# Kernel optimization log

Measured on AMD Instinct MI355X. Metric: run time of the kernel, lower is better.

The kernel has to match this reference:

```python
import jax, jax.numpy as jnp
import numpy as np

T_DIFF = 1000.0
LN_EPS = 1e-5


def _lin(x, w, b):
    return jnp.matmul(x, w.T) + b


def _ln(x, g, b):
    m = jnp.mean(x, axis=-1, keepdims=True)
    v = jnp.mean((x - m) ** 2, axis=-1, keepdims=True)
    return (x - m) / jnp.sqrt(v + LN_EPS) * g + b


def _pos_lin(x, w, b):
    return jnp.matmul(x, jax.nn.softplus(w).T) + b


def _gamma(t, g_l1_w, g_l1_b, g_l2_w, g_l2_b, g_l3_w, g_l3_b, gamma_0, gamma_1):
    def gtilde(u):
        l1 = _pos_lin(u, g_l1_w, g_l1_b)
        return l1 + _pos_lin(jax.nn.sigmoid(_pos_lin(l1, g_l2_w, g_l2_b)), g_l3_w, g_l3_b)
    g0, g1, gt = gtilde(jnp.zeros_like(t)), gtilde(jnp.ones_like(t)), gtilde(t)
    return gamma_0 + (gamma_1 - gamma_0) * (gt - g0) / (g1 - g0)


def _pair_dist(a):
    # safe pairwise euclidean distances, (B,N,N,1)
    diff = a[:, :, None, :] - a[:, None, :, :]
    d2 = jnp.sum(diff * diff, axis=-1, keepdims=True)
    return diff, jnp.sqrt(jnp.maximum(d2, 1e-12)), d2


def _egc_layer(x, h, x0, p):
    _, d0, _ = _pair_dist(x0)                      # original distances
    diff, dist, d2 = _pair_dist(x)                 # current distances (pre-LN x)
    h = _ln(h, p['lnh_g'], p['lnh_b'])
    x = _ln(x, p['lnx_g'], p['lnx_b'])
    B, N, F = h.shape
    h_i = jnp.broadcast_to(h[:, :, None, :], (B, N, N, F))
    h_j = jnp.broadcast_to(h[:, None, :, :], (B, N, N, F))
    einp = jnp.concatenate([h_i, h_j, d2, d0], axis=-1)  # (B,N,N,2F+2)
    m = jax.nn.silu(_lin(einp, p['edg1_w'], p['edg1_b']))
    m = jax.nn.silu(_lin(m, p['edg2_w'], p['edg2_b']))
    e = jax.nn.sigmoid(_lin(m, p['edgi_w'], p['edgi_b']))
    e = e * (1.0 - jnp.eye(N, dtype=e.dtype)[None, :, :, None])
    m_agg = jnp.sum(e * m, axis=2)                 # sum over j -> (B,N,F)
    hn = jax.nn.silu(_lin(jnp.concatenate([h, m_agg], axis=-1), p['node1_w'], p['node1_b']))
    hn = h + _lin(hn, p['node2_w'], p['node2_b'])
    cw = jax.nn.silu(_lin(einp, p['cor1_w'], p['cor1_b']))
    cw = jax.nn.silu(_lin(cw, p['cor2_w'], p['cor2_b']))
    cw = _lin(cw, p['cor3_w'], p['cor3_b'])        # (B,N,N,1)
    x_next = x + jnp.sum(cw * (diff / (dist + 1.0)), axis=2)
    return x_next, hn


def setup_inputs() -> dict:
    key = jax.random.key(0)
    ks = iter(jax.random.split(key, 64))
    B, N, H, L = 8, 192, 32, 4
    d = {}
    d['xyz_atom_species'] = jax.random.normal(next(ks), (B, N, 4), jnp.float32)
    d['pdf'] = jax.random.normal(next(ks), (B, 3000), jnp.float32)
    d['t'] = jax.random.uniform(next(ks), (B,), jnp.float32) * T_DIFF

    def w(k, shape):
        fan_in = shape[-1]
        return jax.random.normal(k, shape, jnp.float32) / np.sqrt(fan_in)

    d['emb_in_w'] = w(next(ks), (H, 12)); d['emb_in_b'] = jnp.zeros((H,), jnp.float32)
    d['emb_out_w'] = w(next(ks), (1, H)); d['emb_out_b'] = jnp.zeros((1,), jnp.float32)
    d['x_out_w'] = w(next(ks), (3, 3)); d['x_out_b'] = jnp.zeros((3,), jnp.float32)
    d['pdf_w'] = w(next(ks), (10, 3000)); d['pdf_b'] = jnp.zeros((10,), jnp.float32)
    d['g_l1_w'] = w(next(ks), (1, 1)); d['g_l1_b'] = jnp.zeros((1,), jnp.float32)
    d['g_l2_w'] = w(next(ks), (1024, 1)); d['g_l2_b'] = jnp.zeros((1024,), jnp.float32)
    d['g_l3_w'] = w(next(ks), (1, 1024)); d['g_l3_b'] = jnp.zeros((1,), jnp.float32)
    d['gamma_0'] = jnp.array([-5.0], jnp.float32)
    d['gamma_1'] = jnp.array([10.0], jnp.float32)
    d['lnh_g'] = jnp.ones((L, H), jnp.float32); d['lnh_b'] = jnp.zeros((L, H), jnp.float32)
    d['lnx_g'] = jnp.ones((L, 3), jnp.float32); d['lnx_b'] = jnp.zeros((L, 3), jnp.float32)
    d['edg1_w'] = w(next(ks), (L, H, 2 * H + 2)); d['edg1_b'] = jnp.zeros((L, H), jnp.float32)
    d['edg2_w'] = w(next(ks), (L, H, H)); d['edg2_b'] = jnp.zeros((L, H), jnp.float32)
    d['edgi_w'] = w(next(ks), (L, 1, H)); d['edgi_b'] = jnp.zeros((L, 1), jnp.float32)
    d['node1_w'] = w(next(ks), (L, H, 2 * H)); d['node1_b'] = jnp.zeros((L, H), jnp.float32)
    d['node2_w'] = w(next(ks), (L, H, H)); d['node2_b'] = jnp.zeros((L, H), jnp.float32)
    d['cor1_w'] = w(next(ks), (L, H, 2 * H + 2)); d['cor1_b'] = jnp.zeros((L, H), jnp.float32)
    d['cor2_w'] = w(next(ks), (L, H, H)); d['cor2_b'] = jnp.zeros((L, H), jnp.float32)
    d['cor3_w'] = w(next(ks), (L, 1, H)); d['cor3_b'] = jnp.zeros((L, 1), jnp.float32)
    return d


def reference(xyz_atom_species, pdf, t, emb_in_w, emb_in_b, emb_out_w, emb_out_b,
              x_out_w, x_out_b, pdf_w, pdf_b, g_l1_w, g_l1_b, g_l2_w, g_l2_b,
              g_l3_w, g_l3_b, gamma_0, gamma_1, lnh_g, lnh_b, lnx_g, lnx_b,
              edg1_w, edg1_b, edg2_w, edg2_b, edgi_w, edgi_b, node1_w, node1_b,
              node2_w, node2_b, cor1_w, cor1_b, cor2_w, cor2_b, cor3_w, cor3_b):
    B, N, _ = xyz_atom_species.shape
    h = xyz_atom_species[:, :, 3:4]                # (B,N,1)
    x = xyz_atom_species[:, :, :3]
    x0 = x
    tn = (t / T_DIFF)[:, None]                     # (B,1)
    t_emb = _gamma(tn, g_l1_w, g_l1_b, g_l2_w, g_l2_b, g_l3_w, g_l3_b, gamma_0, gamma_1)
    pdf_emb = _lin(pdf, pdf_w, pdf_b)              # (B,10)
    h = jnp.concatenate([
        h,
        jnp.broadcast_to(t_emb[:, None, :], (B, N, 1)),
        jnp.broadcast_to(pdf_emb[:, None, :], (B, N, 10)),
    ], axis=-1)
    h = _lin(h, emb_in_w, emb_in_b)                # (B,N,32)
    for l in range(4):
        p = dict(lnh_g=lnh_g[l], lnh_b=lnh_b[l], lnx_g=lnx_g[l], lnx_b=lnx_b[l],
                 edg1_w=edg1_w[l], edg1_b=edg1_b[l], edg2_w=edg2_w[l], edg2_b=edg2_b[l],
                 edgi_w=edgi_w[l], edgi_b=edgi_b[l], node1_w=node1_w[l], node1_b=node1_b[l],
                 node2_w=node2_w[l], node2_b=node2_b[l], cor1_w=cor1_w[l], cor1_b=cor1_b[l],
                 cor2_w=cor2_w[l], cor2_b=cor2_b[l], cor3_w=cor3_w[l], cor3_b=cor3_b[l])
        x, h = _egc_layer(x, h, x0, p)
    h = _lin(h, emb_out_w, emb_out_b)
    x = _lin(x, x_out_w, x_out_b) - x0
    return jnp.concatenate([x, h], axis=-1)        # (B,N,4)
```

## Files before the change

### kernel.cpp

```cpp
#include <hip/hip_runtime.h>
#include <hip/hip_bf16.h>
#include <math.h>

#define BATCH 8
#define NATOMS 192

using short8 = __attribute__((ext_vector_type(8))) short;
using f32x4  = __attribute__((ext_vector_type(4))) float;

__device__ __forceinline__ float fast_rcp(float x){ return __builtin_amdgcn_rcpf(x); }
__device__ __forceinline__ float sigmoid_f(float x){ return fast_rcp(1.0f+__expf(-x)); }
__device__ __forceinline__ float silu_f(float x){ return x*fast_rcp(1.0f+__expf(-x)); }
__device__ __forceinline__ float softplus_f(float x){ return fmaxf(x,0.0f)+log1pf(expf(-fabsf(x))); }
__device__ __forceinline__ unsigned short f2bf(float x){
  __hip_bfloat16 h = __float2bfloat16(x);
  return __builtin_bit_cast(unsigned short, h);
}

__device__ __forceinline__ float wave_sum(float v){
  v += __shfl_xor(v, 1);
  v += __shfl_xor(v, 2);
  v += __shfl_xor(v, 4);
  v += __shfl_xor(v, 8);
  v += __shfl_xor(v, 16);
  v += __shfl_xor(v, 32);
  return v;
}
__device__ __forceinline__ float sum32(float v){
  v += __shfl_xor(v, 1);
  v += __shfl_xor(v, 2);
  v += __shfl_xor(v, 4);
  v += __shfl_xor(v, 8);
  v += __shfl_xor(v, 16);
  return v;
}
__device__ __forceinline__ float sum16(float v){
  v += __shfl_xor(v, 1);
  v += __shfl_xor(v, 2);
  v += __shfl_xor(v, 4);
  v += __shfl_xor(v, 8);
  return v;
}

struct KP {
  const float *xyz, *pdf, *t;
  const float *emb_in_w, *emb_in_b, *emb_out_w, *emb_out_b, *x_out_w, *x_out_b;
  const float *pdf_w, *pdf_b;
  const float *g1w, *g1b, *g2w, *g2b, *g3w, *g3b, *gamma0, *gamma1;
  const float *lnhg, *lnhb, *lnxg, *lnxb;
  const float *e1w, *e1b, *e2w, *e2b, *eiw, *eib;
  const float *n1w, *n1b, *n2w, *n2b;
  const float *c1w, *c1b, *c2w, *c2b, *c3w, *c3b;
  float *temb, *pdfe;
  unsigned short *e2wb, *c2wb;
  float *hln0, *hln1, *ue0, *uc0, *vep0, *vcp0, *ue1, *uc1, *vep1, *vcp1;
  float *xb0, *xb1;
  float *out;
};

__global__ __launch_bounds__(128) void k_prelude(KP P)
{
  __shared__ float s_sm[8];
  const int bx = blockIdx.x, tid = threadIdx.x;
  const int wv = tid >> 6, ln = tid & 63;

  if (bx < 80){
    const int b = bx / 10, o = bx % 10;
    const float* pb = P.pdf + b*3000;
    const float* wb = P.pdf_w + o*3000;
    float p = 0.f;
    for (int k = tid; k < 3000; k += 128) p = fmaf(pb[k], wb[k], p);
    p = wave_sum(p);
    if (ln == 0) s_sm[wv] = p;
    __syncthreads();
    if (tid == 0) P.pdfe[b*10 + o] = s_sm[0] + s_sm[1] + P.pdf_b[o];
  } else if (bx < 88){
    const int b = bx - 80;
    const float w1 = softplus_f(P.g1w[0]);
    const float b1 = P.g1b[0];
    const float tn = P.t[b] * (1.0f/1000.0f);
    const float l1_0 = b1;
    const float l1_1 = w1 + b1;
    const float l1_t = fmaf(w1, tn, b1);
    float a0 = 0.f, a1 = 0.f, at = 0.f;
    for (int k = tid; k < 1024; k += 128){
      float w2 = softplus_f(P.g2w[k]);
      float bb = P.g2b[k];
      float w3 = softplus_f(P.g3w[k]);
      a0 += sigmoid_f(fmaf(w2, l1_0, bb)) * w3;
      a1 += sigmoid_f(fmaf(w2, l1_1, bb)) * w3;
      at += sigmoid_f(fmaf(w2, l1_t, bb)) * w3;
    }
    float vals[3] = {a0, a1, at};
#pragma unroll
    for (int r = 0; r < 3; ++r){
      float v = wave_sum(vals[r]);
      if (ln == 0) s_sm[r*2 + wv] = v;
    }
    __syncthreads();
    if (tid == 0){
      const float b3 = P.g3b[0];
      const float g0  = l1_0 + s_sm[0] + s_sm[1] + b3;
      const float g1v = l1_1 + s_sm[2] + s_sm[3] + b3;
      const float gt  = l1_t + s_sm[4] + s_sm[5] + b3;
      P.temb[b] = P.gamma0[0] + (P.gamma1[0] - P.gamma0[0]) * (gt - g0) / (g1v - g0);
    }
  } else {
    const int g = (bx - 88)*128 + tid;
    P.e2wb[g] = f2bf(P.e2w[g]);
    P.c2wb[g] = f2bf(P.c2w[g]);
  }
}

__global__ __launch_bounds__(128) void k_embed(KP P)
{
  __shared__ float s_hl[32];
  const int nid = blockIdx.x;
  const int tid = threadIdx.x;
  const int wv = tid >> 6, ln = tid & 63;
  const int b = nid / NATOMS;
  if (tid < 32){
    const int f = tid;
    const float* w = P.emb_in_w + f*12;
    float a = P.emb_in_b[f];
    a = fmaf(P.xyz[nid*4 + 3], w[0], a);
    a = fmaf(P.temb[b], w[1], a);
    const float* pe = P.pdfe + b*10;
#pragma unroll
    for (int q = 0; q < 10; ++q) a = fmaf(pe[q], w[2+q], a);
    const float m = sum32(a) * (1.0f/32.0f);
    const float d = a - m;
    const float v = sum32(d*d);
    const float r = rsqrtf(v*(1.0f/32.0f) + 1e-5f);
    const float hlv = fmaf(d*r, P.lnhg[f], P.lnhb[f]);
    s_hl[f] = hlv;
    P.hln0[(size_t)nid*32 + f] = hlv;
    if (f < 3) P.xb0[(size_t)nid*3 + f] = P.xyz[nid*4 + f];
  }
  __syncthreads();
  if (ln < 32){
    const int f = ln;
    const float* W = ((wv == 0) ? P.e1w : P.c1w) + f*66;
    float sv = ((wv == 0) ? P.e1b : P.c1b)[f], su = 0.f;
#pragma unroll
    for (int k = 0; k < 32; ++k){ sv = fmaf(s_hl[k], W[k], sv); su = fmaf(s_hl[k], W[32+k], su); }
    if (wv == 0){ P.vep0[(size_t)nid*32 + f] = sv; P.ue0[(size_t)nid*32 + f] = su; }
    else        { P.vcp0[(size_t)nid*32 + f] = sv; P.uc0[(size_t)nid*32 + f] = su; }
  }
}

__global__ __launch_bounds__(256, 4) void k_layer(KP P, int l, int last,
    const float* __restrict__ xcur, float* __restrict__ xnxt,
    const float* __restrict__ hlnC, float* __restrict__ hlnN,
    const float* __restrict__ ueC, const float* __restrict__ ucC,
    const float* __restrict__ vepC, const float* __restrict__ vcpC,
    float* __restrict__ ueN, float* __restrict__ ucN,
    float* __restrict__ vepN, float* __restrict__ vcpN)
{
  __shared__ float s_geo[192][6];
  __shared__ float s_mgp[2][32];
  __shared__ float s_pxp[2][4];
  __shared__ float s_hv[32];
  __shared__ float s_n1[32];
  __shared__ float s_hl[32];

  const int nid = blockIdx.x;
  const int b = nid / NATOMS;
  const int i = nid - b*NATOMS;
  const int base = b*NATOMS;
  const int tid = threadIdx.x;
  const int wv = tid >> 6, lane = tid & 63;
  const int n16 = lane & 15, quad = lane >> 4;
  const int is_edge = (wv < 2);
  const int half = wv & 1;

  {
    const float* xi_p = xcur + (size_t)nid*3;
    const float xi0 = xi_p[0], xi1 = xi_p[1], xi2 = xi_p[2];
    const float* x0i = P.xyz + (size_t)nid*4;
    const float q0i = x0i[0], q1i = x0i[1], q2i = x0i[2];
    for (int j = tid; j < NATOMS; j += 256){
      const float* xj_p = xcur + (size_t)(base + j)*3;
      const float dfx = xi0 - xj_p[0], dfy = xi1 - xj_p[1], dfz = xi2 - xj_p[2];
      const float d2 = dfx*dfx + dfy*dfy + dfz*dfz;
      const float dist = sqrtf(fmaxf(d2, 1e-12f));
      const float* x0j = P.xyz + (size_t)(base + j)*4;
      const float q0 = q0i - x0j[0], q1 = q1i - x0j[1], q2 = q2i - x0j[2];
      const float d0 = sqrtf(fmaxf(q0*q0 + q1*q1 + q2*q2, 1e-12f));
      s_geo[j][0] = dfx; s_geo[j][1] = dfy; s_geo[j][2] = dfz;
      s_geo[j][3] = d2;  s_geo[j][4] = d0;  s_geo[j][5] = dist;
    }
  }

  const float* e1wl = (is_edge ? P.e1w : P.c1w) + l*2112;
  const float* vp   = (is_edge ? vepC : vcpC) + (size_t)nid*32;
  const float* uu   = is_edge ? ueC : ucC;
  const unsigned short* w2b = (is_edge ? P.e2wb : P.c2wb) + l*1024;
  const float* bias2 = (is_edge ? P.e2b : P.c2b) + l*32;
  const float* wout  = (is_edge ? P.eiw : P.c3w) + l*32;
  const float  bout  = (is_edge ? P.eib : P.c3b)[l];

  float vp8[8], wA[8], wB[8];
#pragma unroll
  for (int q = 0; q < 8; ++q){
    const int k = quad*8 + q;
    vp8[q] = vp[k];
    wA[q] = e1wl[k*66 + 64];
    wB[q] = e1wl[k*66 + 65];
  }
  const short8 wb0 = *(const short8*)(w2b + n16*32 + quad*8);
  const short8 wb1 = *(const short8*)(w2b + 512 + n16*32 + quad*8);

  float bA[4], bB[4], wAo[4], wBo[4];
#pragma unroll
  for (int r = 0; r < 4; ++r){
    bA[r]  = bias2[quad*4 + r];
    bB[r]  = bias2[16 + quad*4 + r];
    wAo[r] = wout[quad*4 + r];
    wBo[r] = wout[16 + quad*4 + r];
  }

  __syncthreads();

  float acc0[4] = {0.f,0.f,0.f,0.f};
  float acc1[4] = {0.f,0.f,0.f,0.f};
  float px = 0.f, py = 0.f, pz = 0.f;

#pragma unroll 3
  for (int t = half; t < 12; t += 2){
    const int j = t*16 + n16;
    const float d2 = s_geo[j][3], d0 = s_geo[j][4];
    const float* ur = uu + (size_t)(base + j)*32 + quad*8;
    const f32x4 ua = *(const f32x4*)ur;
    const f32x4 ub = *(const f32x4*)(ur + 4);
    short8 a;
#pragma unroll
    for (int q = 0; q < 4; ++q)
      a[q] = (short)f2bf(silu_f(fmaf(d2, wA[q], fmaf(d0, wB[q], vp8[q] + ua[q]))));
#pragma unroll
    for (int q = 0; q < 4; ++q)
      a[4+q] = (short)f2bf(silu_f(fmaf(d2, wA[4+q], fmaf(d0, wB[4+q], vp8[4+q] + ub[q]))));

    const f32x4 z = {0.f, 0.f, 0.f, 0.f};
    const f32x4 A0 = __builtin_amdgcn_mfma_f32_16x16x32_bf16(wb0, a, z, 0, 0, 0);
    const f32x4 A1 = __builtin_amdgcn_mfma_f32_16x16x32_bf16(wb1, a, z, 0, 0, 0);

    float m20[4], m21[4];
#pragma unroll
    for (int r = 0; r < 4; ++r){
      m20[r] = silu_f(A0[r] + bA[r]);
      m21[r] = silu_f(A1[r] + bB[r]);
    }
    float gp = 0.f;
#pragma unroll
    for (int r = 0; r < 4; ++r) gp += m20[r]*wAo[r] + m21[r]*wBo[r];
    gp += __shfl_xor(gp, 16);
    gp += __shfl_xor(gp, 32);

    if (is_edge){
      const float e = (j == i) ? 0.0f : sigmoid_f(gp + bout);
#pragma unroll
      for (int r = 0; r < 4; ++r){
        acc0[r] = fmaf(e, m20[r], acc0[r]);
        acc1[r] = fmaf(e, m21[r], acc1[r]);
      }
    } else {
      const float s = (gp + bout) * fast_rcp(s_geo[j][5] + 1.0f);
      px = fmaf(s, s_geo[j][0], px);
      py = fmaf(s, s_geo[j][1], py);
      pz = fmaf(s, s_geo[j][2], pz);
    }
  }

  if (is_edge){
#pragma unroll
    for (int r = 0; r < 4; ++r){
      acc0[r] = sum16(acc0[r]);
      acc1[r] = sum16(acc1[r]);
    }
    if (n16 == 0){
#pragma unroll
      for (int r = 0; r < 4; ++r){
        s_mgp[half][quad*4 + r] = acc0[r];
        s_mgp[half][16 + quad*4 + r] = acc1[r];
      }
    }
  } else {
    px = sum16(px); py = sum16(py); pz = sum16(pz);
    if (lane == 0){
      s_pxp[half][0] = px; s_pxp[half][1] = py; s_pxp[half][2] = pz;
    }
    if (half == 1 && lane < 32) s_hv[lane] = hlnC[(size_t)nid*32 + lane];
  }
  __syncthreads();

  if (wv == 0){
    if (lane < 32){
      const int f = lane;
      float a = P.n1b[l*32 + f];
      const float* w1 = P.n1w + l*2048 + f*64;
#pragma unroll
      for (int k = 0; k < 32; ++k) a = fmaf(s_hv[k], w1[k], a);
#pragma unroll
      for (int k = 0; k < 32; ++k) a = fmaf(s_mgp[0][k] + s_mgp[1][k], w1[32+k], a);
      s_n1[f] = silu_f(a);
    }
  } else if (wv == 1){
    const float tx = s_pxp[0][0] + s_pxp[1][0];
    const float ty = s_pxp[0][1] + s_pxp[1][1];
    const float tz = s_pxp[0][2] + s_pxp[1][2];
    const float* xr = xcur + (size_t)nid*3;
    const float x0 = xr[0], x1 = xr[1], x2 = xr[2];
    const float mx = (x0 + x1 + x2) * (1.0f/3.0f);
    const float v0 = x0-mx, v1 = x1-mx, v2 = x2-mx;
    const float r = rsqrtf((v0*v0 + v1*v1 + v2*v2)*(1.0f/3.0f) + 1e-5f);
    const float xn0 = fmaf((x0 - mx)*r, P.lnxg[l*3+0], P.lnxb[l*3+0]) + tx;
    const float xn1 = fmaf((x1 - mx)*r, P.lnxg[l*3+1], P.lnxb[l*3+1]) + ty;
    const float xn2 = fmaf((x2 - mx)*r, P.lnxg[l*3+2], P.lnxb[l*3+2]) + tz;
    if (!last){
      if (lane == 0){
        float* xo = xnxt + (size_t)nid*3;
        xo[0] = xn0; xo[1] = xn1; xo[2] = xn2;
      }
    } else if (lane < 3){
      const float xn[3] = {xn0, xn1, xn2};
      float o = P.x_out_b[lane];
      o = fmaf(xn[0], P.x_out_w[lane*3 + 0], o);
      o = fmaf(xn[1], P.x_out_w[lane*3 + 1], o);
      o = fmaf(xn[2], P.x_out_w[lane*3 + 2], o);
      P.out[(size_t)nid*4 + lane] = o - P.xyz[(size_t)nid*4 + lane];
    }
  }
  __syncthreads();

  if (wv == 0 && lane < 32){
    const int f = lane;
    float o = P.n2b[l*32 + f];
    const float* w2 = P.n2w + l*1024 + f*32;
#pragma unroll
    for (int k = 0; k < 32; ++k) o = fmaf(s_n1[k], w2[k], o);
    const float ho = s_hv[f] + o;
    if (last){
      float hp = sum32(ho * P.emb_out_w[f]);
      if (f == 0) P.out[(size_t)nid*4 + 3] = hp + P.emb_out_b[0];
    } else {
      const int nx = l + 1;
      const float m = sum32(ho) * (1.0f/32.0f);
      const float d = ho - m;
      const float v = sum32(d*d);
      const float r = rsqrtf(v*(1.0f/32.0f) + 1e-5f);
      const float hlv = fmaf(d*r, P.lnhg[nx*32 + f], P.lnhb[nx*32 + f]);
      s_hl[f] = hlv;
      hlnN[(size_t)nid*32 + f] = hlv;
    }
  }
  if (!last){
    __syncthreads();
    if (wv < 2 && lane < 32){
      const int f = lane;
      const int nx = l + 1;
      const float* W = ((wv == 0) ? P.e1w : P.c1w) + nx*2112 + f*66;
      float sv = ((wv == 0) ? P.e1b : P.c1b)[nx*32 + f], su = 0.f;
#pragma unroll
      for (int k = 0; k < 32; ++k){ sv = fmaf(s_hl[k], W[k], sv); su = fmaf(s_hl[k], W[32+k], su); }
      if (wv == 0){ vepN[(size_t)nid*32 + f] = sv; ueN[(size_t)nid*32 + f] = su; }
      else        { vcpN[(size_t)nid*32 + f] = sv; ucN[(size_t)nid*32 + f] = su; }
    }
  }
}

extern "C" void kernel_launch(void* const* d_in, const int* in_sizes, int n_in,
                              void* d_out, int out_size, void* d_ws, size_t ws_size,
                              hipStream_t stream)
{
  const int NTOT = BATCH*NATOMS;
  float* ws   = (float*)d_ws;

  KP P;
  P.xyz      = (const float*)d_in[0];
  P.pdf      = (const float*)d_in[1];
  P.t        = (const float*)d_in[2];
  P.emb_in_w = (const float*)d_in[3];
  P.emb_in_b = (const float*)d_in[4];
  P.emb_out_w= (const float*)d_in[5];
  P.emb_out_b= (const float*)d_in[6];
  P.x_out_w  = (const float*)d_in[7];
  P.x_out_b  = (const float*)d_in[8];
  P.pdf_w    = (const float*)d_in[9];
  P.pdf_b    = (const float*)d_in[10];
  P.g1w      = (const float*)d_in[11];
  P.g1b      = (const float*)d_in[12];
  P.g2w      = (const float*)d_in[13];
  P.g2b      = (const float*)d_in[14];
  P.g3w      = (const float*)d_in[15];
  P.g3b      = (const float*)d_in[16];
  P.gamma0   = (const float*)d_in[17];
  P.gamma1   = (const float*)d_in[18];
  P.lnhg     = (const float*)d_in[19];
  P.lnhb     = (const float*)d_in[20];
  P.lnxg     = (const float*)d_in[21];
  P.lnxb     = (const float*)d_in[22];
  P.e1w      = (const float*)d_in[23];
  P.e1b      = (const float*)d_in[24];
  P.e2w      = (const float*)d_in[25];
  P.e2b      = (const float*)d_in[26];
  P.eiw      = (const float*)d_in[27];
  P.eib      = (const float*)d_in[28];
  P.n1w      = (const float*)d_in[29];
  P.n1b      = (const float*)d_in[30];
  P.n2w      = (const float*)d_in[31];
  P.n2b      = (const float*)d_in[32];
  P.c1w      = (const float*)d_in[33];
  P.c1b      = (const float*)d_in[34];
  P.c2w      = (const float*)d_in[35];
  P.c2b      = (const float*)d_in[36];
  P.c3w      = (const float*)d_in[37];
  P.c3b      = (const float*)d_in[38];

  P.temb = ws;
  P.pdfe = ws + 8;
  P.e2wb = (unsigned short*)(ws + 96);
  P.c2wb = P.e2wb + 4096;
  float* p = ws + 96 + 4096;
  P.hln0 = p; p += NTOT*32;
  P.hln1 = p; p += NTOT*32;
  P.ue0  = p; p += NTOT*32;
  P.uc0  = p; p += NTOT*32;
  P.vep0 = p; p += NTOT*32;
  P.vcp0 = p; p += NTOT*32;
  P.ue1  = p; p += NTOT*32;
  P.uc1  = p; p += NTOT*32;
  P.vep1 = p; p += NTOT*32;
  P.vcp1 = p; p += NTOT*32;
  P.xb0  = p; p += NTOT*3;
  P.xb1  = p; p += NTOT*3;
  P.out  = (float*)d_out;

  k_prelude<<<120, 128, 0, stream>>>(P);
  k_embed<<<NTOT, 128, 0, stream>>>(P);

  float* xcur = P.xb0; float* xnxt = P.xb1;
  float* hlnC = P.hln0; float* hlnN = P.hln1;
  float* ueC = P.ue0;  float* ucC = P.uc0;  float* vepC = P.vep0; float* vcpC = P.vcp0;
  float* ueN = P.ue1;  float* ucN = P.uc1;  float* vepN = P.vep1; float* vcpN = P.vcp1;
  for (int l = 0; l < 4; ++l){
    k_layer<<<NTOT, 256, 0, stream>>>(P, l, (l == 3) ? 1 : 0, xcur, xnxt,
        hlnC, hlnN, ueC, ucC, vepC, vcpC, ueN, ucN, vepN, vcpN);
    float* tp;
    tp = hlnC; hlnC = hlnN; hlnN = tp;
    tp = ueC;  ueC  = ueN;  ueN  = tp;
    tp = ucC;  ucC  = ucN;  ucN  = tp;
    tp = vepC; vepC = vepN; vepN = tp;
    tp = vcpC; vcpC = vcpN; vcpN = tp;
    tp = xcur; xcur = xnxt; xnxt = tp;
  }
}
```

Before: 235.6 us.

## Double waves per layer block and fold bias into MFMA accumulator

The per-atom layer kernel now runs 512 threads: four waves do edge work and four do coordinate work, each handling three neighbor tiles instead of six. The second-layer bias is passed as the MFMA accumulator input instead of being added afterwards. The shared geometry array is padded to eight floats so d2/d0 and the displacement/distance values load as vectors, and d2/d0 are preloaded before the loop. This aims to cut the serial loop length per wave and hide latency better, at the cost of more partial sums to combine, idle waves during the node update, and register pressure from the new launch bounds.

```diff
diff --git a/kernel.cpp b/kernel.cpp
--- a/kernel.cpp
+++ b/kernel.cpp
@@ -4,6 +4,7 @@
 
 #define BATCH 8
 #define NATOMS 192
+#define NTOT (BATCH*NATOMS)
 
 using short8 = __attribute__((ext_vector_type(8))) short;
 using f32x4  = __attribute__((ext_vector_type(4))) float;
@@ -149,7 +150,7 @@
   }
 }
 
-__global__ __launch_bounds__(256, 4) void k_layer(KP P, int l, int last,
+__global__ __launch_bounds__(512, 6) void k_layer(KP P, int l, int last,
     const float* __restrict__ xcur, float* __restrict__ xnxt,
     const float* __restrict__ hlnC, float* __restrict__ hlnN,
     const float* __restrict__ ueC, const float* __restrict__ ucC,
@@ -157,9 +158,9 @@
     float* __restrict__ ueN, float* __restrict__ ucN,
     float* __restrict__ vepN, float* __restrict__ vcpN)
 {
-  __shared__ float s_geo[192][6];
-  __shared__ float s_mgp[2][32];
-  __shared__ float s_pxp[2][4];
+  __shared__ float s_geo[192][8];
+  __shared__ float s_mgp[4][32];
+  __shared__ float s_pxp[4][4];
   __shared__ float s_hv[32];
   __shared__ float s_n1[32];
   __shared__ float s_hl[32];
@@ -171,15 +172,15 @@
   const int tid = threadIdx.x;
   const int wv = tid >> 6, lane = tid & 63;
   const int n16 = lane & 15, quad = lane >> 4;
-  const int is_edge = (wv < 2);
-  const int half = wv & 1;
+  const int is_edge = (wv < 4);
+  const int sub = wv & 3;
 
   {
     const float* xi_p = xcur + (size_t)nid*3;
     const float xi0 = xi_p[0], xi1 = xi_p[1], xi2 = xi_p[2];
     const float* x0i = P.xyz + (size_t)nid*4;
     const float q0i = x0i[0], q1i = x0i[1], q2i = x0i[2];
-    for (int j = tid; j < NATOMS; j += 256){
+    for (int j = tid; j < NATOMS; j += 512){
       const float* xj_p = xcur + (size_t)(base + j)*3;
       const float dfx = xi0 - xj_p[0], dfy = xi1 - xj_p[1], dfz = xi2 - xj_p[2];
       const float d2 = dfx*dfx + dfy*dfy + dfz*dfz;
@@ -187,8 +188,8 @@
       const float* x0j = P.xyz + (size_t)(base + j)*4;
       const float q0 = q0i - x0j[0], q1 = q1i - x0j[1], q2 = q2i - x0j[2];
       const float d0 = sqrtf(fmaxf(q0*q0 + q1*q1 + q2*q2, 1e-12f));
-      s_geo[j][0] = dfx; s_geo[j][1] = dfy; s_geo[j][2] = dfz;
-      s_geo[j][3] = d2;  s_geo[j][4] = d0;  s_geo[j][5] = dist;
+      s_geo[j][0] = d2;  s_geo[j][1] = d0;
+      s_geo[j][4] = dfx; s_geo[j][5] = dfy; s_geo[j][6] = dfz; s_geo[j][7] = dist;
     }
   }
 
@@ -211,28 +212,41 @@
   const short8 wb0 = *(const short8*)(w2b + n16*32 + quad*8);
   const short8 wb1 = *(const short8*)(w2b + 512 + n16*32 + quad*8);
 
-  float bA[4], bB[4], wAo[4], wBo[4];
+  f32x4 cb0, cb1;
+  float wAo[4], wBo[4];
 #pragma unroll
   for (int r = 0; r < 4; ++r){
-    bA[r]  = bias2[quad*4 + r];
-    bB[r]  = bias2[16 + quad*4 + r];
+    cb0[r] = bias2[quad*4 + r];
+    cb1[r] = bias2[16 + quad*4 + r];
     wAo[r] = wout[quad*4 + r];
     wBo[r] = wout[16 + quad*4 + r];
   }
 
   __syncthreads();
+
+  float gd2[3], gd0[3];
+#pragma unroll
+  for (int r3 = 0; r3 < 3; ++r3){
+    const int j = (sub + r3*4)*16 + n16;
+    const float2 dd = *(const float2*)&s_geo[j][0];
+    gd2[r3] = dd.x; gd0[r3] = dd.y;
+  }
+
+  const float* up = uu + base*32;
+  int uoff = (sub*16 + n16)*32 + quad*8;
 
   float acc0[4] = {0.f,0.f,0.f,0.f};
   float acc1[4] = {0.f,0.f,0.f,0.f};
   float px = 0.f, py = 0.f, pz = 0.f;
 
-#pragma unroll 3
-  for (int t = half; t < 12; t += 2){
+#pragma unroll
+  for (int r3 = 0; r3 < 3; ++r3){
+    const int t = sub + r3*4;
     const int j = t*16 + n16;
-    const float d2 = s_geo[j][3], d0 = s_geo[j][4];
-    const float* ur = uu + (size_t)(base + j)*32 + quad*8;
-    const f32x4 ua = *(const f32x4*)ur;
-    const f32x4 ub = *(const f32x4*)(ur + 4);
+    const f32x4 ua = *(const f32x4*)(up + uoff);
+    const f32x4 ub = *(const f32x4*)(up + uoff + 4);
+    uoff += 2048;
+    const float d2 = gd2[r3], d0 = gd0[r3];
     short8 a;
 #pragma unroll
     for (int q = 0; q < 4; ++q)
@@ -241,15 +255,14 @@
     for (int q = 0; q < 4; ++q)
       a[4+q] = (short)f2bf(silu_f(fmaf(d2, wA[4+q], fmaf(d0, wB[4+q], vp8[4+q] + ub[q]))));
 
-    const f32x4 z = {0.f, 0.f, 0.f, 0.f};
-    const f32x4 A0 = __builtin_amdgcn_mfma_f32_16x16x32_bf16(wb0, a, z, 0, 0, 0);
-    const f32x4 A1 = __builtin_amdgcn_mfma_f32_16x16x32_bf16(wb1, a, z, 0, 0, 0);
+    const f32x4 A0 = __builtin_amdgcn_mfma_f32_16x16x32_bf16(wb0, a, cb0, 0, 0, 0);
+    const f32x4 A1 = __builtin_amdgcn_mfma_f32_16x16x32_bf16(wb1, a, cb1, 0, 0, 0);
 
     float m20[4], m21[4];
 #pragma unroll
     for (int r = 0; r < 4; ++r){
-      m20[r] = silu_f(A0[r] + bA[r]);
-      m21[r] = silu_f(A1[r] + bB[r]);
+      m20[r] = silu_f(A0[r]);
+      m21[r] = silu_f(A1[r]);
     }
     float gp = 0.f;
 #pragma unroll
@@ -265,10 +278,11 @@
         acc1[r] = fmaf(e, m21[r], acc1[r]);
       }
     } else {
-      const float s = (gp + bout) * fast_rcp(s_geo[j][5] + 1.0f);
-      px = fmaf(s, s_geo[j][0], px);
-      py = fmaf(s, s_geo[j][1], py);
-      pz = fmaf(s, s_geo[j][2], pz);
+      const f32x4 gv = *(const f32x4*)&s_geo[j][4];
+      const float s = (gp + bout) * fast_rcp(gv[3] + 1.0f);
+      px = fmaf(s, gv[0], px);
+      py = fmaf(s, gv[1], py);
+      pz = fmaf(s, gv[2], pz);
     }
   }
 
@@ -281,16 +295,16 @@
     if (n16 == 0){
 #pragma unroll
       for (int r = 0; r < 4; ++r){
-        s_mgp[half][quad*4 + r] = acc0[r];
-        s_mgp[half][16 + quad*4 + r] = acc1[r];
+        s_mgp[sub][quad*4 + r] = acc0[r];
+        s_mgp[sub][16 + quad*4 + r] = acc1[r];
       }
     }
   } else {
     px = sum16(px); py = sum16(py); pz = sum16(pz);
     if (lane == 0){
-      s_pxp[half][0] = px; s_pxp[half][1] = py; s_pxp[half][2] = pz;
-    }
-    if (half == 1 && lane < 32) s_hv[lane] = hlnC[(size_t)nid*32 + lane];
+      s_pxp[sub][0] = px; s_pxp[sub][1] = py; s_pxp[sub][2] = pz;
+    }
+    if (sub == 3 && lane < 32) s_hv[lane] = hlnC[(size_t)nid*32 + lane];
   }
   __syncthreads();
 
@@ -302,13 +316,14 @@
 #pragma unroll
       for (int k = 0; k < 32; ++k) a = fmaf(s_hv[k], w1[k], a);
 #pragma unroll
-      for (int k = 0; k < 32; ++k) a = fmaf(s_mgp[0][k] + s_mgp[1][k], w1[32+k], a);
+      for (int k = 0; k < 32; ++k)
+        a = fmaf(s_mgp[0][k] + s_mgp[1][k] + s_mgp[2][k] + s_mgp[3][k], w1[32+k], a);
       s_n1[f] = silu_f(a);
     }
   } else if (wv == 1){
-    const float tx = s_pxp[0][0] + s_pxp[1][0];
-    const float ty = s_pxp[0][1] + s_pxp[1][1];
-    const float tz = s_pxp[0][2] + s_pxp[1][2];
+    const float tx = s_pxp[0][0] + s_pxp[1][0] + s_pxp[2][0] + s_pxp[3][0];
+    const float ty = s_pxp[0][1] + s_pxp[1][1] + s_pxp[2][1] + s_pxp[3][1];
+    const float tz = s_pxp[0][2] + s_pxp[1][2] + s_pxp[2][2] + s_pxp[3][2];
     const float* xr = xcur + (size_t)nid*3;
     const float x0 = xr[0], x1 = xr[1], x2 = xr[2];
     const float mx = (x0 + x1 + x2) * (1.0f/3.0f);
@@ -373,7 +388,6 @@
                               void* d_out, int out_size, void* d_ws, size_t ws_size,
                               hipStream_t stream)
 {
-  const int NTOT = BATCH*NATOMS;
   float* ws   = (float*)d_ws;
 
   KP P;
@@ -444,7 +458,7 @@
   float* ueC = P.ue0;  float* ucC = P.uc0;  float* vepC = P.vep0; float* vcpC = P.vcp0;
   float* ueN = P.ue1;  float* ucN = P.uc1;  float* vepN = P.vep1; float* vcpN = P.vcp1;
   for (int l = 0; l < 4; ++l){
-    k_layer<<<NTOT, 256, 0, stream>>>(P, l, (l == 3) ? 1 : 0, xcur, xnxt,
+    k_layer<<<NTOT, 512, 0, stream>>>(P, l, (l == 3) ? 1 : 0, xcur, xnxt,
         hlnC, hlnN, ueC, ucC, vepC, vcpC, ueN, ucN, vepN, vcpN);
     float* tp;
     tp = hlnC; hlnC = hlnN; hlnN = tp;
```

Measured after the change: 302.0 us. 1.28x slower.

## Prefetch u rows, split geometry into SoA LDS, fold bias into MFMA

Applied to the files above, without the earlier changes.

Rewrites the per-atom layer kernel's edge loop so each iteration loads the next tile's u rows before the current tile is computed, and fully unrolls the loop. The interleaved geometry array is split into separate per-field shared arrays, and the geometry setup loop becomes a single guarded assignment per thread. The second-layer bias is passed as the MFMA accumulator instead of being added afterwards. Launch bounds rise from 4 to 6 blocks per CU, which may squeeze registers and cause spills given the extra prefetch registers.

```diff
diff --git a/kernel.cpp b/kernel.cpp
--- a/kernel.cpp
+++ b/kernel.cpp
@@ -4,6 +4,7 @@
 
 #define BATCH 8
 #define NATOMS 192
+#define NTOT (BATCH*NATOMS)
 
 using short8 = __attribute__((ext_vector_type(8))) short;
 using f32x4  = __attribute__((ext_vector_type(4))) float;
@@ -149,7 +150,7 @@
   }
 }
 
-__global__ __launch_bounds__(256, 4) void k_layer(KP P, int l, int last,
+__global__ __launch_bounds__(256, 6) void k_layer(KP P, int l, int last,
     const float* __restrict__ xcur, float* __restrict__ xnxt,
     const float* __restrict__ hlnC, float* __restrict__ hlnN,
     const float* __restrict__ ueC, const float* __restrict__ ucC,
@@ -157,7 +158,8 @@
     float* __restrict__ ueN, float* __restrict__ ucN,
     float* __restrict__ vepN, float* __restrict__ vcpN)
 {
-  __shared__ float s_geo[192][6];
+  __shared__ float s_d2[192], s_d0[192];
+  __shared__ float s_dfx[192], s_dfy[192], s_dfz[192], s_dist[192];
   __shared__ float s_mgp[2][32];
   __shared__ float s_pxp[2][4];
   __shared__ float s_hv[32];
@@ -174,22 +176,21 @@
   const int is_edge = (wv < 2);
   const int half = wv & 1;
 
-  {
+  if (tid < NATOMS){
+    const int j = tid;
     const float* xi_p = xcur + (size_t)nid*3;
     const float xi0 = xi_p[0], xi1 = xi_p[1], xi2 = xi_p[2];
     const float* x0i = P.xyz + (size_t)nid*4;
     const float q0i = x0i[0], q1i = x0i[1], q2i = x0i[2];
-    for (int j = tid; j < NATOMS; j += 256){
-      const float* xj_p = xcur + (size_t)(base + j)*3;
-      const float dfx = xi0 - xj_p[0], dfy = xi1 - xj_p[1], dfz = xi2 - xj_p[2];
-      const float d2 = dfx*dfx + dfy*dfy + dfz*dfz;
-      const float dist = sqrtf(fmaxf(d2, 1e-12f));
-      const float* x0j = P.xyz + (size_t)(base + j)*4;
-      const float q0 = q0i - x0j[0], q1 = q1i - x0j[1], q2 = q2i - x0j[2];
-      const float d0 = sqrtf(fmaxf(q0*q0 + q1*q1 + q2*q2, 1e-12f));
-      s_geo[j][0] = dfx; s_geo[j][1] = dfy; s_geo[j][2] = dfz;
-      s_geo[j][3] = d2;  s_geo[j][4] = d0;  s_geo[j][5] = dist;
-    }
+    const float* xj_p = xcur + (size_t)(base + j)*3;
+    const float dfx = xi0 - xj_p[0], dfy = xi1 - xj_p[1], dfz = xi2 - xj_p[2];
+    const float d2 = dfx*dfx + dfy*dfy + dfz*dfz;
+    const float dist = sqrtf(fmaxf(d2, 1e-12f));
+    const float* x0j = P.xyz + (size_t)(base + j)*4;
+    const float q0 = q0i - x0j[0], q1 = q1i - x0j[1], q2 = q2i - x0j[2];
+    const float d0 = sqrtf(fmaxf(q0*q0 + q1*q1 + q2*q2, 1e-12f));
+    s_d2[j] = d2;  s_d0[j] = d0;
+    s_dfx[j] = dfx; s_dfy[j] = dfy; s_dfz[j] = dfz; s_dist[j] = dist;
   }
 
   const float* e1wl = (is_edge ? P.e1w : P.c1w) + l*2112;
@@ -211,11 +212,12 @@
   const short8 wb0 = *(const short8*)(w2b + n16*32 + quad*8);
   const short8 wb1 = *(const short8*)(w2b + 512 + n16*32 + quad*8);
 
-  float bA[4], bB[4], wAo[4], wBo[4];
+  f32x4 cb0, cb1;
+  float wAo[4], wBo[4];
 #pragma unroll
   for (int r = 0; r < 4; ++r){
-    bA[r]  = bias2[quad*4 + r];
-    bB[r]  = bias2[16 + quad*4 + r];
+    cb0[r] = bias2[quad*4 + r];
+    cb1[r] = bias2[16 + quad*4 + r];
     wAo[r] = wout[quad*4 + r];
     wBo[r] = wout[16 + quad*4 + r];
   }
@@ -226,30 +228,37 @@
   float acc1[4] = {0.f,0.f,0.f,0.f};
   float px = 0.f, py = 0.f, pz = 0.f;
 
-#pragma unroll 3
-  for (int t = half; t < 12; t += 2){
+  const float* up = uu + base*32;
+  int uoff = (half*16 + n16)*32 + quad*8;
+  f32x4 cua = *(const f32x4*)(up + uoff);
+  f32x4 cub = *(const f32x4*)(up + uoff + 4);
+#pragma unroll
+  for (int it = 0; it < 6; ++it){
+    const int t = half + it*2;
     const int j = t*16 + n16;
-    const float d2 = s_geo[j][3], d0 = s_geo[j][4];
-    const float* ur = uu + (size_t)(base + j)*32 + quad*8;
-    const f32x4 ua = *(const f32x4*)ur;
-    const f32x4 ub = *(const f32x4*)(ur + 4);
+    f32x4 nua = cua, nub = cub;
+    if (it < 5){
+      nua = *(const f32x4*)(up + uoff + 1024);
+      nub = *(const f32x4*)(up + uoff + 1024 + 4);
+    }
+    uoff += 1024;
+    const float d2 = s_d2[j], d0 = s_d0[j];
     short8 a;
 #pragma unroll
     for (int q = 0; q < 4; ++q)
-      a[q] = (short)f2bf(silu_f(fmaf(d2, wA[q], fmaf(d0, wB[q], vp8[q] + ua[q]))));
+      a[q] = (short)f2bf(silu_f(fmaf(d2, wA[q], fmaf(d0, wB[q], vp8[q] + cua[q]))));
 #pragma unroll
     for (int q = 0; q < 4; ++q)
-      a[4+q] = (short)f2bf(silu_f(fmaf(d2, wA[4+q], fmaf(d0, wB[4+q], vp8[4+q] + ub[q]))));
-
-    const f32x4 z = {0.f, 0.f, 0.f, 0.f};
-    const f32x4 A0 = __builtin_amdgcn_mfma_f32_16x16x32_bf16(wb0, a, z, 0, 0, 0);
-    const f32x4 A1 = __builtin_amdgcn_mfma_f32_16x16x32_bf16(wb1, a, z, 0, 0, 0);
+      a[4+q] = (short)f2bf(silu_f(fmaf(d2, wA[4+q], fmaf(d0, wB[4+q], vp8[4+q] + cub[q]))));
+
+    const f32x4 A0 = __builtin_amdgcn_mfma_f32_16x16x32_bf16(wb0, a, cb0, 0, 0, 0);
+    const f32x4 A1 = __builtin_amdgcn_mfma_f32_16x16x32_bf16(wb1, a, cb1, 0, 0, 0);
 
     float m20[4], m21[4];
 #pragma unroll
     for (int r = 0; r < 4; ++r){
-      m20[r] = silu_f(A0[r] + bA[r]);
-      m21[r] = silu_f(A1[r] + bB[r]);
+      m20[r] = silu_f(A0[r]);
+      m21[r] = silu_f(A1[r]);
     }
     float gp = 0.f;
 #pragma unroll
@@ -265,11 +274,12 @@
         acc1[r] = fmaf(e, m21[r], acc1[r]);
       }
     } else {
-      const float s = (gp + bout) * fast_rcp(s_geo[j][5] + 1.0f);
-      px = fmaf(s, s_geo[j][0], px);
-      py = fmaf(s, s_geo[j][1], py);
-      pz = fmaf(s, s_geo[j][2], pz);
-    }
+      const float s = (gp + bout) * fast_rcp(s_dist[j] + 1.0f);
+      px = fmaf(s, s_dfx[j], px);
+      py = fmaf(s, s_dfy[j], py);
+      pz = fmaf(s, s_dfz[j], pz);
+    }
+    cua = nua; cub = nub;
   }
 
   if (is_edge){
@@ -373,7 +383,6 @@
                               void* d_out, int out_size, void* d_ws, size_t ws_size,
                               hipStream_t stream)
 {
-  const int NTOT = BATCH*NATOMS;
   float* ws   = (float*)d_ws;
 
   KP P;
```

After: 275.6 us. +17.0%, slower.
